# Kernel tuning notes

Measured on AMD Instinct MI355X. Metric: run time of the kernel, lower is better.

## Reference

```python
import jax, jax.numpy as jnp
import numpy as np

IN_CH = 128
OUT_CH = 128
N_NODES = 20000
N_EDGES = 320000
EPS = 1e-5


def setup_inputs() -> dict:
    key = jax.random.key(0)
    ks = jax.random.split(key, 8)
    node_embeddings = jax.random.normal(ks[0], (N_NODES, IN_CH), dtype=jnp.float32)
    edge_index = jax.random.randint(ks[1], (2, N_EDGES), 0, N_NODES, dtype=jnp.int64)
    s = 1.0 / np.sqrt(IN_CH)
    W1 = jax.random.uniform(ks[2], (IN_CH, IN_CH), jnp.float32, -s, s)
    b1 = jax.random.uniform(ks[3], (IN_CH,), jnp.float32, -s, s)
    W2 = jax.random.uniform(ks[4], (IN_CH, IN_CH), jnp.float32, -s, s)
    b2 = jax.random.uniform(ks[5], (IN_CH,), jnp.float32, -s, s)
    sm = 1.0 / np.sqrt(2 * IN_CH)
    Wm = jax.random.uniform(ks[6], (2 * IN_CH, 2 * OUT_CH), jnp.float32, -sm, sm)
    bm = jax.random.uniform(ks[7], (2 * OUT_CH,), jnp.float32, -sm, sm)
    gamma = jnp.ones((OUT_CH,), jnp.float32)
    beta = jnp.zeros((OUT_CH,), jnp.float32)
    return {"node_embeddings": node_embeddings, "edge_index": edge_index,
            "W1": W1, "b1": b1, "W2": W2, "b2": b2,
            "Wm": Wm, "bm": bm, "gamma": gamma, "beta": beta}


def reference(node_embeddings, edge_index, W1, b1, W2, b2, Wm, bm, gamma, beta):
    # gather endpoint embeddings: [E, d]
    src = node_embeddings[edge_index[0]]
    dst = node_embeddings[edge_index[1]]
    src_emb = src @ W1 + b1                       # Linear v1
    dst_emb = dst @ W2 + b2                       # Linear v2
    edge_attr = jnp.concatenate([src_emb, dst_emb], axis=-1)  # [E, 2d]
    h = edge_attr @ Wm + bm                       # [E, 2*out]
    x, gate = jnp.split(h, 2, axis=-1)            # GeGLU (exact gelu, torch default)
    y = x * jax.nn.gelu(gate, approximate=False)  # [E, out]
    mu = jnp.mean(y, axis=-1, keepdims=True)
    var = jnp.var(y, axis=-1, keepdims=True)
    y_norm = (y - mu) * jax.lax.rsqrt(var + EPS)
    return y_norm * gamma + beta
```

## Files before the change

kernel.cpp:

```cpp
#include <hip/hip_runtime.h>
#include <hip/hip_fp16.h>
#include <math.h>


#define CH 128
#define NB 32
#define BCAP 11264

typedef _Float16 half8 __attribute__((ext_vector_type(8)));
typedef float floatx4 __attribute__((ext_vector_type(4)));

__device__ __forceinline__ int permcol(int j2) {
  int c = j2 & 127;
  int isg = j2 >> 7;
  return ((c >> 1) << 2) | (isg << 1) | (c & 1);
}

__global__ __launch_bounds__(256) void prep_kernel(
    const float* __restrict__ W1, const float* __restrict__ b1,
    const float* __restrict__ W2, const float* __restrict__ b2,
    const float* __restrict__ Wm, const float* __restrict__ bm,
    __half* __restrict__ CcatT, float* __restrict__ dvec,
    unsigned int* __restrict__ cursor) {
  int bid = blockIdx.x;
  int tid = threadIdx.x;
  if (bid < 256) {
    int idx = bid * 256 + tid;
    int i = idx >> 9;
    int j = idx & 511;
    int jc = j & 255;
    const float* wrow = (j < 256) ? (W1 + i * CH) : (W2 + i * CH);
    const float* wm   = (j < 256) ? (Wm + jc) : (Wm + CH * 256 + jc);
    float acc = 0.f;
#pragma unroll 8
    for (int k = 0; k < CH; ++k) acc = fmaf(wrow[k], wm[k * 256], acc);
    int scol = (j & 256) | permcol(j & 255);
    CcatT[scol * CH + i] = __float2half(acc);
  } else if (tid < 256) {
    if (tid < NB) cursor[tid] = (unsigned int)tid * BCAP;
    float acc = bm[tid];
#pragma unroll 8
    for (int k = 0; k < CH; ++k) {
      acc = fmaf(b1[k], Wm[k * 256 + tid], acc);
      acc = fmaf(b2[k], Wm[(CH + k) * 256 + tid], acc);
    }
    dvec[permcol(tid)] = acc;
  }
}

#define SCHUNK 2048
__global__ __launch_bounds__(256) void scatter_kernel(
    const int* __restrict__ eidx, int E, int npb,
    unsigned int* __restrict__ cursor,
    int* __restrict__ sorted_e, int2* __restrict__ sorted_sd) {
  __shared__ unsigned int lcnt[NB], lbase[NB], loff[NB];
  __shared__ signed char lkey[SCHUNK];
  const int tid = threadIdx.x;
  const int c0 = blockIdx.x * SCHUNK;
  if (tid < NB) { lcnt[tid] = 0; loff[tid] = 0; }
  __syncthreads();
  for (int i = tid; i < SCHUNK; i += 256) {
    int e = c0 + i;
    int k = -1;
    if (e < E) { int s = eidx[e]; k = s / npb; atomicAdd(&lcnt[k], 1u); }
    lkey[i] = (signed char)k;
  }
  __syncthreads();
  if (tid < NB) {
    unsigned int c = lcnt[tid];
    lbase[tid] = c ? atomicAdd(&cursor[tid], c) : 0u;
  }
  __syncthreads();
  for (int i = tid; i < SCHUNK; i += 256) {
    int e = c0 + i;
    if (e < E) {
      int k = (int)lkey[i];
      unsigned int r = atomicAdd(&loff[k], 1u);
      unsigned int pos = lbase[k] + r;
      sorted_e[pos] = e;
      sorted_sd[pos] = make_int2(eidx[e], eidx[E + e]);
    }
  }
}

__global__ __launch_bounds__(256) void node_gemm(
    const float* __restrict__ A,
    const __half* __restrict__ BT,
    __half* __restrict__ C,
    int M) {
  __shared__ __align__(16) _Float16 As[64 * 136];
  __shared__ __align__(16) _Float16 Bs[64 * 136];
  const int tid = threadIdx.x;
  const int row0 = blockIdx.x * 64;
  const int col0 = blockIdx.y * 64;

#pragma unroll
  for (int rnd = 0; rnd < 4; ++rnd) {
    int idx = (tid + rnd * 256) * 8;
    int r = idx >> 7, c = idx & 127;
    int rg = row0 + r; if (rg >= M) rg = M - 1;
    float4 v0 = *(const float4*)(A + (size_t)rg * CH + c);
    float4 v1 = *(const float4*)(A + (size_t)rg * CH + c + 4);
    __half2 h0 = __floats2half2_rn(v0.x, v0.y);
    __half2 h1 = __floats2half2_rn(v0.z, v0.w);
    __half2 h2 = __floats2half2_rn(v1.x, v1.y);
    __half2 h3 = __floats2half2_rn(v1.z, v1.w);
    uint4 u;
    u.x = *(const unsigned int*)&h0; u.y = *(const unsigned int*)&h1;
    u.z = *(const unsigned int*)&h2; u.w = *(const unsigned int*)&h3;
    *(uint4*)(As + r * 136 + c) = u;
    uint4 w4 = *(const uint4*)(BT + (size_t)(col0 + r) * CH + c);
    *(uint4*)(Bs + r * 136 + c) = w4;
  }
  __syncthreads();

  const int w = tid >> 6, l = tid & 63;
  const int mr = w * 16 + (l & 15);
  const int kq = (l >> 4) * 8;

  half8 a[4];
#pragma unroll
  for (int kc = 0; kc < 4; ++kc)
    a[kc] = *(const half8*)(As + mr * 136 + kc * 32 + kq);

  floatx4 acc[4] = {{0,0,0,0},{0,0,0,0},{0,0,0,0},{0,0,0,0}};
#pragma unroll
  for (int kc = 0; kc < 4; ++kc) {
#pragma unroll
    for (int nb = 0; nb < 4; ++nb) {
      half8 b = *(const half8*)(Bs + (nb * 16 + (l & 15)) * 136 + kc * 32 + kq);
      acc[nb] = __builtin_amdgcn_mfma_f32_16x16x32_f16(a[kc], b, acc[nb], 0, 0, 0);
    }
  }

  const int colb = col0 + (l & 15);
  const int rowb = row0 + w * 16 + (l >> 4) * 4;
#pragma unroll
  for (int nb = 0; nb < 4; ++nb) {
#pragma unroll
    for (int rg = 0; rg < 4; ++rg) {
      int row = rowb + rg;
      if (row < M)
        C[(size_t)row * 512 + colb + nb * 16] = __float2half(acc[nb][rg]);
    }
  }
}

__device__ __forceinline__ float gelu_t(float g) {
  float g2 = g * g;
  float t = g * fmaf(g2, 0.10294515f, 2.3021858f);
  float u = exp2f(t);
  return g * u * __builtin_amdgcn_rcpf(1.0f + u);
}

__device__ __forceinline__ void process_edge(
    uint4 pu, uint4 qu, float4 dv0, float4 dv1, float4 gm, float4 bt,
    float* __restrict__ outp, int hl) {
  float2 px01 = __half22float2(*(const __half2*)&pu.x);
  float2 pg01 = __half22float2(*(const __half2*)&pu.y);
  float2 px23 = __half22float2(*(const __half2*)&pu.z);
  float2 pg23 = __half22float2(*(const __half2*)&pu.w);
  float2 qx01 = __half22float2(*(const __half2*)&qu.x);
  float2 qg01 = __half22float2(*(const __half2*)&qu.y);
  float2 qx23 = __half22float2(*(const __half2*)&qu.z);
  float2 qg23 = __half22float2(*(const __half2*)&qu.w);

  float x0 = px01.x + qx01.x + dv0.x;
  float x1 = px01.y + qx01.y + dv0.y;
  float g0 = pg01.x + qg01.x + dv0.z;
  float g1 = pg01.y + qg01.y + dv0.w;
  float x2 = px23.x + qx23.x + dv1.x;
  float x3 = px23.y + qx23.y + dv1.y;
  float g2 = pg23.x + qg23.x + dv1.z;
  float g3 = pg23.y + qg23.y + dv1.w;

  float y0 = x0 * gelu_t(g0);
  float y1 = x1 * gelu_t(g1);
  float y2 = x2 * gelu_t(g2);
  float y3 = x3 * gelu_t(g3);

  float s1 = (y0 + y1) + (y2 + y3);
  float s2 = fmaf(y0, y0, fmaf(y1, y1, fmaf(y2, y2, y3 * y3)));
#pragma unroll
  for (int off = 16; off; off >>= 1) {
    s1 += __shfl_xor(s1, off, 64);
    s2 += __shfl_xor(s2, off, 64);
  }
  float mu  = s1 * (1.0f / 128.0f);
  float var = s2 * (1.0f / 128.0f) - mu * mu;
  float rstd = rsqrtf(var + 1e-5f);

  float4 o;
  o.x = fmaf((y0 - mu) * rstd, gm.x, bt.x);
  o.y = fmaf((y1 - mu) * rstd, gm.y, bt.y);
  o.z = fmaf((y2 - mu) * rstd, gm.z, bt.z);
  o.w = fmaf((y3 - mu) * rstd, gm.w, bt.w);
  *(float4*)(outp + hl * 4) = o;
}

__global__ __launch_bounds__(256) void edge_kernel(
    const __half* __restrict__ PQ,
    const float* __restrict__ dvec,
    const float* __restrict__ gamma,
    const float* __restrict__ beta,
    const unsigned int* __restrict__ cursor,
    const int* __restrict__ sorted_e,
    const int2* __restrict__ sorted_sd,
    float* __restrict__ out) {
  const int per = gridDim.x >> 3;
  const int nb2 = (blockIdx.x & 7) * per + (blockIdx.x >> 3);
  const int wave = threadIdx.x >> 6;
  const int lane = threadIdx.x & 63;
  const int hl = lane & 31;
  const int side = lane >> 5;
  const int i0 = nb2 * 16 + wave * 4 + side;

  const int slotA = i0, slotB = i0 + 2;
  const int bA = slotA / BCAP, bB = slotB / BCAP;
  const bool vA = (unsigned int)slotA < cursor[bA];
  const bool vB = (unsigned int)slotB < cursor[bB];
  if (!vA && !vB) return;

  float4 dv0 = *(const float4*)(dvec + hl * 8);
  float4 dv1 = *(const float4*)(dvec + hl * 8 + 4);
  float4 gm  = *(const float4*)(gamma + hl * 4);
  float4 bt  = *(const float4*)(beta + hl * 4);

  int eA = 0, sA = 0, dA = 0, eB = 0, sB = 0, dB = 0;
  if (vA) { eA = sorted_e[slotA]; int2 sd = sorted_sd[slotA]; sA = sd.x; dA = sd.y; }
  if (vB) { eB = sorted_e[slotB]; int2 sd = sorted_sd[slotB]; sB = sd.x; dB = sd.y; }

  const char* pqb = (const char*)PQ;
  uint4 puA = *(const uint4*)(pqb + (size_t)sA * 1024 + hl * 16);
  uint4 quA = *(const uint4*)(pqb + (size_t)dA * 1024 + 512 + hl * 16);
  uint4 puB = *(const uint4*)(pqb + (size_t)sB * 1024 + hl * 16);
  uint4 quB = *(const uint4*)(pqb + (size_t)dB * 1024 + 512 + hl * 16);

  if (vA)
    process_edge(puA, quA, dv0, dv1, gm, bt, out + (size_t)eA * CH, hl);
  if (vB)
    process_edge(puB, quB, dv0, dv1, gm, bt, out + (size_t)eB * CH, hl);
}

extern "C" void kernel_launch(void* const* d_in, const int* in_sizes, int n_in,
                              void* d_out, int out_size, void* d_ws, size_t ws_size,
                              hipStream_t stream) {
  const float* emb   = (const float*)d_in[0];
  const int*   eidx  = (const int*)d_in[1];
  const float* W1    = (const float*)d_in[2];
  const float* b1    = (const float*)d_in[3];
  const float* W2    = (const float*)d_in[4];
  const float* b2    = (const float*)d_in[5];
  const float* Wm    = (const float*)d_in[6];
  const float* bm    = (const float*)d_in[7];
  const float* gamma = (const float*)d_in[8];
  const float* beta  = (const float*)d_in[9];

  const int M = in_sizes[0] / CH;
  const int E = in_sizes[1] / 2;
  const int npb = (M + NB - 1) / NB;

  float*        dvec      = (float*)d_ws;
  unsigned int* cursor    = (unsigned int*)(dvec + 256);
  __half*       CcatT     = (__half*)(cursor + 64);
  int*          sorted_e  = (int*)(CcatT + 512 * CH);
  int2*         sorted_sd = (int2*)(sorted_e + NB * BCAP);
  __half*       PQ        = (__half*)(sorted_sd + NB * BCAP);

  prep_kernel<<<257, 256, 0, stream>>>(W1, b1, W2, b2, Wm, bm, CcatT, dvec,
                                       cursor);

  scatter_kernel<<<(E + SCHUNK - 1) / SCHUNK, 256, 0, stream>>>(
      eidx, E, npb, cursor, sorted_e, sorted_sd);

  dim3 g2((M + 63) / 64, 512 / 64);
  node_gemm<<<g2, 256, 0, stream>>>(emb, CcatT, PQ, M);

  const int nslots = NB * BCAP;
  edge_kernel<<<nslots / 16, 256, 0, stream>>>(PQ, dvec, gamma, beta, cursor,
                                               sorted_e, sorted_sd,
                                               (float*)d_out);
}
```

Baseline: 93.07 us.

## Fuse prep and scatter kernels, pack sorted edge records, add halves in fp16

Merges the weight-folding prep kernel and the edge bucketing scatter into one launch, with cursors zeroed by a memset and bucket offsets made relative. Sorted edge records become a single int2 holding the edge id plus 15-bit src/dst packed together, which removes one array and one load per edge. The scatter keeps src/dst in registers instead of reloading eidx, and the P+Q sum is done in half2 before converting to float. BCAP is shrunk to cut the edge kernel's grid. The risks are reduced precision from the fp16 add, the 15-bit packing that only holds for fewer than 32768 nodes, and bucket overflow if a bucket ever exceeds the smaller capacity.

```diff
diff --git a/kernel.cpp b/kernel.cpp
--- a/kernel.cpp
+++ b/kernel.cpp
@@ -5,7 +5,8 @@
 
 #define CH 128
 #define NB 32
-#define BCAP 11264
+#define BCAP 10496
+#define SCHUNK 2048
 
 typedef _Float16 half8 __attribute__((ext_vector_type(8)));
 typedef float floatx4 __attribute__((ext_vector_type(4)));
@@ -16,14 +17,16 @@
   return ((c >> 1) << 2) | (isg << 1) | (c & 1);
 }
 
-__global__ __launch_bounds__(256) void prep_kernel(
+__global__ __launch_bounds__(256) void prep_scatter_kernel(
     const float* __restrict__ W1, const float* __restrict__ b1,
     const float* __restrict__ W2, const float* __restrict__ b2,
     const float* __restrict__ Wm, const float* __restrict__ bm,
     __half* __restrict__ CcatT, float* __restrict__ dvec,
-    unsigned int* __restrict__ cursor) {
-  int bid = blockIdx.x;
-  int tid = threadIdx.x;
+    const int* __restrict__ eidx, int E, int npb,
+    unsigned int* __restrict__ cursor,
+    int2* __restrict__ sorted) {
+  const int bid = blockIdx.x;
+  const int tid = threadIdx.x;
   if (bid < 256) {
     int idx = bid * 256 + tid;
     int i = idx >> 9;
@@ -36,49 +39,51 @@
     for (int k = 0; k < CH; ++k) acc = fmaf(wrow[k], wm[k * 256], acc);
     int scol = (j & 256) | permcol(j & 255);
     CcatT[scol * CH + i] = __float2half(acc);
-  } else if (tid < 256) {
-    if (tid < NB) cursor[tid] = (unsigned int)tid * BCAP;
-    float acc = bm[tid];
+    return;
+  }
+  if (bid == 256) {
+    if (tid < 256) {
+      float acc = bm[tid];
 #pragma unroll 8
-    for (int k = 0; k < CH; ++k) {
-      acc = fmaf(b1[k], Wm[k * 256 + tid], acc);
-      acc = fmaf(b2[k], Wm[(CH + k) * 256 + tid], acc);
-    }
-    dvec[permcol(tid)] = acc;
-  }
-}
-
-#define SCHUNK 2048
-__global__ __launch_bounds__(256) void scatter_kernel(
-    const int* __restrict__ eidx, int E, int npb,
-    unsigned int* __restrict__ cursor,
-    int* __restrict__ sorted_e, int2* __restrict__ sorted_sd) {
+      for (int k = 0; k < CH; ++k) {
+        acc = fmaf(b1[k], Wm[k * 256 + tid], acc);
+        acc = fmaf(b2[k], Wm[(CH + k) * 256 + tid], acc);
+      }
+      dvec[permcol(tid)] = acc;
+    }
+    return;
+  }
   __shared__ unsigned int lcnt[NB], lbase[NB], loff[NB];
-  __shared__ signed char lkey[SCHUNK];
-  const int tid = threadIdx.x;
-  const int c0 = blockIdx.x * SCHUNK;
+  const int c0 = (bid - 257) * SCHUNK;
   if (tid < NB) { lcnt[tid] = 0; loff[tid] = 0; }
   __syncthreads();
-  for (int i = tid; i < SCHUNK; i += 256) {
-    int e = c0 + i;
-    int k = -1;
-    if (e < E) { int s = eidx[e]; k = s / npb; atomicAdd(&lcnt[k], 1u); }
-    lkey[i] = (signed char)k;
+  int svals[SCHUNK / 256], dvals[SCHUNK / 256];
+  signed char kvals[SCHUNK / 256];
+#pragma unroll
+  for (int r = 0; r < SCHUNK / 256; ++r) {
+    int e = c0 + r * 256 + tid;
+    int k = -1, s = 0, d = 0;
+    if (e < E) {
+      s = eidx[e]; d = eidx[E + e];
+      k = s / npb;
+      atomicAdd(&lcnt[k], 1u);
+    }
+    svals[r] = s; dvals[r] = d; kvals[r] = (signed char)k;
   }
   __syncthreads();
   if (tid < NB) {
     unsigned int c = lcnt[tid];
-    lbase[tid] = c ? atomicAdd(&cursor[tid], c) : 0u;
-  }
-  __syncthreads();
-  for (int i = tid; i < SCHUNK; i += 256) {
-    int e = c0 + i;
+    lbase[tid] = c ? ((unsigned int)tid * BCAP + atomicAdd(&cursor[tid], c))
+                   : 0u;
+  }
+  __syncthreads();
+#pragma unroll
+  for (int r = 0; r < SCHUNK / 256; ++r) {
+    int e = c0 + r * 256 + tid;
     if (e < E) {
-      int k = (int)lkey[i];
-      unsigned int r = atomicAdd(&loff[k], 1u);
-      unsigned int pos = lbase[k] + r;
-      sorted_e[pos] = e;
-      sorted_sd[pos] = make_int2(eidx[e], eidx[E + e]);
+      int k = (int)kvals[r];
+      unsigned int pos = lbase[k] + atomicAdd(&loff[k], 1u);
+      sorted[pos] = make_int2(e, svals[r] | (dvals[r] << 15));
     }
   }
 }
@@ -156,23 +161,19 @@
 __device__ __forceinline__ void process_edge(
     uint4 pu, uint4 qu, float4 dv0, float4 dv1, float4 gm, float4 bt,
     float* __restrict__ outp, int hl) {
-  float2 px01 = __half22float2(*(const __half2*)&pu.x);
-  float2 pg01 = __half22float2(*(const __half2*)&pu.y);
-  float2 px23 = __half22float2(*(const __half2*)&pu.z);
-  float2 pg23 = __half22float2(*(const __half2*)&pu.w);
-  float2 qx01 = __half22float2(*(const __half2*)&qu.x);
-  float2 qg01 = __half22float2(*(const __half2*)&qu.y);
-  float2 qx23 = __half22float2(*(const __half2*)&qu.z);
-  float2 qg23 = __half22float2(*(const __half2*)&qu.w);
-
-  float x0 = px01.x + qx01.x + dv0.x;
-  float x1 = px01.y + qx01.y + dv0.y;
-  float g0 = pg01.x + qg01.x + dv0.z;
-  float g1 = pg01.y + qg01.y + dv0.w;
-  float x2 = px23.x + qx23.x + dv1.x;
-  float x3 = px23.y + qx23.y + dv1.y;
-  float g2 = pg23.x + qg23.x + dv1.z;
-  float g3 = pg23.y + qg23.y + dv1.w;
+  __half2 sx01 = __hadd2(*(const __half2*)&pu.x, *(const __half2*)&qu.x);
+  __half2 sg01 = __hadd2(*(const __half2*)&pu.y, *(const __half2*)&qu.y);
+  __half2 sx23 = __hadd2(*(const __half2*)&pu.z, *(const __half2*)&qu.z);
+  __half2 sg23 = __hadd2(*(const __half2*)&pu.w, *(const __half2*)&qu.w);
+  float2 x01 = __half22float2(sx01);
+  float2 g01 = __half22float2(sg01);
+  float2 x23 = __half22float2(sx23);
+  float2 g23 = __half22float2(sg23);
+
+  float x0 = x01.x + dv0.x, x1 = x01.y + dv0.y;
+  float g0 = g01.x + dv0.z, g1 = g01.y + dv0.w;
+  float x2 = x23.x + dv1.x, x3 = x23.y + dv1.y;
+  float g2 = g23.x + dv1.z, g3 = g23.y + dv1.w;
 
   float y0 = x0 * gelu_t(g0);
   float y1 = x1 * gelu_t(g1);
@@ -204,8 +205,7 @@
     const float* __restrict__ gamma,
     const float* __restrict__ beta,
     const unsigned int* __restrict__ cursor,
-    const int* __restrict__ sorted_e,
-    const int2* __restrict__ sorted_sd,
+    const int2* __restrict__ sorted,
     float* __restrict__ out) {
   const int per = gridDim.x >> 3;
   const int nb2 = (blockIdx.x & 7) * per + (blockIdx.x >> 3);
@@ -217,8 +217,8 @@
 
   const int slotA = i0, slotB = i0 + 2;
   const int bA = slotA / BCAP, bB = slotB / BCAP;
-  const bool vA = (unsigned int)slotA < cursor[bA];
-  const bool vB = (unsigned int)slotB < cursor[bB];
+  const bool vA = (unsigned int)(slotA - bA * BCAP) < cursor[bA];
+  const bool vB = (unsigned int)(slotB - bB * BCAP) < cursor[bB];
   if (!vA && !vB) return;
 
   float4 dv0 = *(const float4*)(dvec + hl * 8);
@@ -227,8 +227,8 @@
   float4 bt  = *(const float4*)(beta + hl * 4);
 
   int eA = 0, sA = 0, dA = 0, eB = 0, sB = 0, dB = 0;
-  if (vA) { eA = sorted_e[slotA]; int2 sd = sorted_sd[slotA]; sA = sd.x; dA = sd.y; }
-  if (vB) { eB = sorted_e[slotB]; int2 sd = sorted_sd[slotB]; sB = sd.x; dB = sd.y; }
+  if (vA) { int2 pk = sorted[slotA]; eA = pk.x; sA = pk.y & 0x7fff; dA = pk.y >> 15; }
+  if (vB) { int2 pk = sorted[slotB]; eB = pk.x; sB = pk.y & 0x7fff; dB = pk.y >> 15; }
 
   const char* pqb = (const char*)PQ;
   uint4 puA = *(const uint4*)(pqb + (size_t)sA * 1024 + hl * 16);
@@ -260,24 +260,22 @@
   const int E = in_sizes[1] / 2;
   const int npb = (M + NB - 1) / NB;
 
-  float*        dvec      = (float*)d_ws;
-  unsigned int* cursor    = (unsigned int*)(dvec + 256);
-  __half*       CcatT     = (__half*)(cursor + 64);
-  int*          sorted_e  = (int*)(CcatT + 512 * CH);
-  int2*         sorted_sd = (int2*)(sorted_e + NB * BCAP);
-  __half*       PQ        = (__half*)(sorted_sd + NB * BCAP);
-
-  prep_kernel<<<257, 256, 0, stream>>>(W1, b1, W2, b2, Wm, bm, CcatT, dvec,
-                                       cursor);
-
-  scatter_kernel<<<(E + SCHUNK - 1) / SCHUNK, 256, 0, stream>>>(
-      eidx, E, npb, cursor, sorted_e, sorted_sd);
+  float*        dvec   = (float*)d_ws;
+  unsigned int* cursor = (unsigned int*)(dvec + 256);
+  __half*       CcatT  = (__half*)(cursor + 64);
+  int2*         sorted = (int2*)(CcatT + 512 * CH);
+  __half*       PQ     = (__half*)(sorted + NB * BCAP);
+
+  hipMemsetAsync(cursor, 0, NB * sizeof(unsigned int), stream);
+
+  const int nchunks = (E + SCHUNK - 1) / SCHUNK;
+  prep_scatter_kernel<<<257 + nchunks, 256, 0, stream>>>(
+      W1, b1, W2, b2, Wm, bm, CcatT, dvec, eidx, E, npb, cursor, sorted);
 
   dim3 g2((M + 63) / 64, 512 / 64);
   node_gemm<<<g2, 256, 0, stream>>>(emb, CcatT, PQ, M);
 
   const int nslots = NB * BCAP;
   edge_kernel<<<nslots / 16, 256, 0, stream>>>(PQ, dvec, gamma, beta, cursor,
-                                               sorted_e, sorted_sd,
-                                               (float*)d_out);
-}
+                                               sorted, (float*)d_out);
+}
```

After: 85.82 us. 1.08x faster.
